# Performance work log

Hardware: AMD Instinct MI355X
Metric: run time of the kernel (lower is better)

Reference implementation:

```python
import jax, jax.numpy as jnp
import numpy as np


def setup_inputs() -> dict:
    key = jax.random.key(0)
    k1, k2, k3 = jax.random.split(key, 3)
    B, C, K, W, H = 8, 512, 512, 64, 64
    x = jax.random.normal(k1, (B, C, W, H), dtype=jnp.float32)
    y = jax.random.normal(k2, (B, K, W, H), dtype=jnp.float32)
    scale = jax.random.uniform(k3, (1,), dtype=jnp.float32)
    return {"x": x, "y": y, "scale": scale}


def reference(x, y, scale):
    B, C, W, H = x.shape
    K = y.shape[1]
    xq = x.reshape(B, C, W * H)            # [B, C, N]
    yk = y.reshape(B, K, W * H)            # [B, K, N]
    # energy = Q @ K^T : [B, C, K]
    energy = jnp.einsum('bcn,bkn->bck', xq, yk)
    # inverted max-subtract softmax over last dim (K)
    energy_new = jnp.max(energy, axis=-1, keepdims=True) - energy
    attention = jax.nn.softmax(energy_new, axis=-1)  # [B, C, K]
    # out = attention @ V : [B, C, N]
    out = jnp.einsum('bck,bkn->bcn', attention, yk).reshape(B, C, W, H)
    return x + scale * out
```

## Files before the change

kernel.cpp:

```cpp
#include <hip/hip_runtime.h>
#include <hip/hip_bf16.h>
#include <stdint.h>

#define BB 8
#define CC 512
#define KK 512
#define NN 4096

typedef __bf16 bf16x8 __attribute__((ext_vector_type(8)));
typedef float f32x4 __attribute__((ext_vector_type(4)));
typedef __attribute__((address_space(3))) uint8_t* lds_ptr_t;
typedef const __attribute__((address_space(1))) uint8_t* gbl_ptr_t;

static __device__ __forceinline__ unsigned short bf16_bits(float f) {
    __bf16 h = (__bf16)f;
    return __builtin_bit_cast(unsigned short, h);
}

__global__ void __launch_bounds__(256) split_hi_lo(const float* __restrict__ in,
        unsigned short* __restrict__ hi, unsigned short* __restrict__ lo, int n4) {
    int idx = blockIdx.x * blockDim.x + threadIdx.x;
    int stride = gridDim.x * blockDim.x;
    const float4* in4 = (const float4*)in;
    ushort4* h4 = (ushort4*)hi;
    ushort4* l4 = (ushort4*)lo;
    for (int i = idx; i < n4; i += stride) {
        float4 v = in4[i];
        float a[4] = {v.x, v.y, v.z, v.w};
        unsigned short hb[4], lb[4];
        #pragma unroll
        for (int j = 0; j < 4; ++j) {
            __bf16 h = (__bf16)a[j];
            float hf = (float)h;
            __bf16 l = (__bf16)(a[j] - hf);
            hb[j] = __builtin_bit_cast(unsigned short, h);
            lb[j] = __builtin_bit_cast(unsigned short, l);
        }
        h4[i] = make_ushort4(hb[0], hb[1], hb[2], hb[3]);
        l4[i] = make_ushort4(lb[0], lb[1], lb[2], lb[3]);
    }
}

__global__ void __launch_bounds__(256) split_y_T(const float* __restrict__ y,
        unsigned short* __restrict__ yh, unsigned short* __restrict__ yl,
        unsigned short* __restrict__ yT) {
    __shared__ unsigned short tile[64][66];
    const int n0 = blockIdx.x * 64, k0 = blockIdx.y * 64, b = blockIdx.z;
    const int t = threadIdx.x;
    const float* src = y + (size_t)b * KK * NN;
    unsigned short* dsth = yh + (size_t)b * KK * NN;
    unsigned short* dstl = yl + (size_t)b * KK * NN;
    unsigned short* dstT = yT + (size_t)b * NN * KK;
    #pragma unroll
    for (int i = 0; i < 4; ++i) {
        int idx = t + 256 * i;
        int r = idx >> 4;
        int c4 = (idx & 15) * 4;
        float4 v = *(const float4*)(src + (size_t)(k0 + r) * NN + n0 + c4);
        float a[4] = {v.x, v.y, v.z, v.w};
        unsigned short hb[4], lb[4];
        #pragma unroll
        for (int q = 0; q < 4; ++q) {
            __bf16 h = (__bf16)a[q];
            float hf = (float)h;
            __bf16 l = (__bf16)(a[q] - hf);
            hb[q] = __builtin_bit_cast(unsigned short, h);
            lb[q] = __builtin_bit_cast(unsigned short, l);
            tile[r][c4 + q] = hb[q];
        }
        size_t off = (size_t)(k0 + r) * NN + n0 + c4;
        *(ushort4*)(dsth + off) = make_ushort4(hb[0], hb[1], hb[2], hb[3]);
        *(ushort4*)(dstl + off) = make_ushort4(lb[0], lb[1], lb[2], lb[3]);
    }
    __syncthreads();
    #pragma unroll
    for (int i = 0; i < 16; ++i) {
        int idx = t + 256 * i;
        int rn = idx >> 6;
        int ck = idx & 63;
        dstT[(size_t)(n0 + rn) * KK + k0 + ck] = tile[ck][rn];
    }
}

__global__ void __launch_bounds__(256) energy_gemm(
        const unsigned short* __restrict__ xh, const unsigned short* __restrict__ xl,
        const unsigned short* __restrict__ yh, const unsigned short* __restrict__ yl,
        float* __restrict__ epart) {
    __shared__ __align__(16) uint8_t smem[4 * 16384];
    const int j = blockIdx.x;
    const int xcd = j & 7;
    const int rem = j >> 3;
    const int ktile = rem & 3;
    const int ctile = (rem >> 2) & 3;
    const int sgrp = rem >> 4;
    const int slice = xcd + 8 * sgrp;
    const int b = slice >> 2;
    const int quarter = slice & 3;
    const int t = threadIdx.x;
    const int wave = t >> 6, lane = t & 63;

    const size_t rowB = (size_t)NN * 2;
    const uint8_t* srcBase[4];
    srcBase[0] = (const uint8_t*)xh + ((size_t)b * CC + ctile * 128) * rowB + (size_t)quarter * 2048;
    srcBase[1] = (const uint8_t*)xl + ((size_t)b * CC + ctile * 128) * rowB + (size_t)quarter * 2048;
    srcBase[2] = (const uint8_t*)yh + ((size_t)b * KK + ktile * 128) * rowB + (size_t)quarter * 2048;
    srcBase[3] = (const uint8_t*)yl + ((size_t)b * KK + ktile * 128) * rowB + (size_t)quarter * 2048;

    f32x4 acc[4][4] = {};
    const int waveRow = wave >> 1, waveCol = wave & 1;

    for (int step = 0; step < 16; ++step) {
        const size_t colByte = (size_t)step * 128;
        #pragma unroll
        for (int i = 0; i < 16; ++i) {
            const int tile = i >> 2;
            const int lc = (i & 3) * 4 + wave;
            const int u = lc * 64 + lane;
            const int r = u >> 3;
            const int c3 = (u & 7) ^ (r & 7);
            const uint8_t* src = srcBase[tile] + (size_t)r * rowB + colByte + c3 * 16;
            __builtin_amdgcn_global_load_lds((gbl_ptr_t)src,
                (lds_ptr_t)(smem + tile * 16384 + lc * 1024), 16, 0, 0);
        }
        __syncthreads();
        #pragma unroll
        for (int kf = 0; kf < 2; ++kf) {
            bf16x8 fah[4], fal[4], fbh[4], fbl[4];
            #pragma unroll
            for (int m = 0; m < 4; ++m) {
                int r = waveRow * 64 + m * 16 + (lane & 15);
                int c3 = (kf * 4 + (lane >> 4)) ^ (r & 7);
                fah[m] = *(const bf16x8*)(smem + 0 * 16384 + r * 128 + c3 * 16);
                fal[m] = *(const bf16x8*)(smem + 1 * 16384 + r * 128 + c3 * 16);
            }
            #pragma unroll
            for (int n = 0; n < 4; ++n) {
                int r = waveCol * 64 + n * 16 + (lane & 15);
                int c3 = (kf * 4 + (lane >> 4)) ^ (r & 7);
                fbh[n] = *(const bf16x8*)(smem + 2 * 16384 + r * 128 + c3 * 16);
                fbl[n] = *(const bf16x8*)(smem + 3 * 16384 + r * 128 + c3 * 16);
            }
            #pragma unroll
            for (int m = 0; m < 4; ++m)
            #pragma unroll
            for (int n = 0; n < 4; ++n) {
                acc[m][n] = __builtin_amdgcn_mfma_f32_16x16x32_bf16(fah[m], fbh[n], acc[m][n], 0, 0, 0);
                acc[m][n] = __builtin_amdgcn_mfma_f32_16x16x32_bf16(fah[m], fbl[n], acc[m][n], 0, 0, 0);
                acc[m][n] = __builtin_amdgcn_mfma_f32_16x16x32_bf16(fal[m], fbh[n], acc[m][n], 0, 0, 0);
            }
        }
        __syncthreads();
    }

    float* eout = epart + (size_t)quarter * BB * CC * KK + (size_t)b * CC * KK;
    const int row0 = ctile * 128 + waveRow * 64;
    const int col0 = ktile * 128 + waveCol * 64;
    #pragma unroll
    for (int m = 0; m < 4; ++m)
    #pragma unroll
    for (int n = 0; n < 4; ++n)
    #pragma unroll
    for (int jj = 0; jj < 4; ++jj) {
        int rr = row0 + m * 16 + (lane >> 4) * 4 + jj;
        int cc2 = col0 + n * 16 + (lane & 15);
        eout[(size_t)rr * KK + cc2] = acc[m][n][jj];
    }
}

__global__ void __launch_bounds__(256) softmax_inv(
        const float* __restrict__ e, unsigned short* __restrict__ att) {
    const int t = threadIdx.x;
    const int wave = t >> 6, lane = t & 63;
    const int row = blockIdx.x * 4 + wave;
    const size_t Q = (size_t)BB * CC * KK;
    const float* p0 = e + (size_t)row * KK;
    float v[8];
    float mn = 3.0e38f;
    #pragma unroll
    for (int i = 0; i < 8; ++i) {
        int c = lane + i * 64;
        v[i] = p0[c] + p0[Q + c] + p0[2 * Q + c] + p0[3 * Q + c];
        mn = fminf(mn, v[i]);
    }
    #pragma unroll
    for (int off = 32; off > 0; off >>= 1) mn = fminf(mn, __shfl_xor(mn, off));
    float p[8]; float s = 0.f;
    #pragma unroll
    for (int i = 0; i < 8; ++i) { p[i] = __expf(mn - v[i]); s += p[i]; }
    #pragma unroll
    for (int off = 32; off > 0; off >>= 1) s += __shfl_xor(s, off);
    float inv = 1.0f / s;
    unsigned short* arow = att + (size_t)row * KK;
    #pragma unroll
    for (int i = 0; i < 8; ++i) arow[lane + i * 64] = bf16_bits(p[i] * inv);
}

__global__ void __launch_bounds__(256) pv_residual(
        const unsigned short* __restrict__ att, const unsigned short* __restrict__ yT,
        const float* __restrict__ x, const float* __restrict__ scale,
        float* __restrict__ out) {
    __shared__ __align__(16) uint8_t smem[2 * 16384];
    const int j = blockIdx.x;
    const int b = j & 7;
    const int rem2 = j >> 3;
    const int ntile = rem2 & 31;
    const int ctile = rem2 >> 5;
    const int t = threadIdx.x;
    const int wave = t >> 6, lane = t & 63;
    const size_t rowB = (size_t)KK * 2;
    const uint8_t* srcA = (const uint8_t*)att + ((size_t)b * CC + ctile * 128) * rowB;
    const uint8_t* srcB = (const uint8_t*)yT  + ((size_t)b * NN + ntile * 128) * rowB;

    f32x4 acc[4][4] = {};
    const int waveRow = wave >> 1, waveCol = wave & 1;

    for (int step = 0; step < 8; ++step) {
        const size_t colByte = (size_t)step * 128;
        #pragma unroll
        for (int i = 0; i < 8; ++i) {
            const uint8_t* base = (i < 4) ? srcA : srcB;
            const int tile = i >> 2;
            const int lc = (i & 3) * 4 + wave;
            const int u = lc * 64 + lane;
            const int r = u >> 3;
            const int c3 = (u & 7) ^ (r & 7);
            const uint8_t* src = base + (size_t)r * rowB + colByte + c3 * 16;
            __builtin_amdgcn_global_load_lds((gbl_ptr_t)src,
                (lds_ptr_t)(smem + tile * 16384 + lc * 1024), 16, 0, 0);
        }
        __syncthreads();
        #pragma unroll
        for (int kf = 0; kf < 2; ++kf) {
            bf16x8 fa[4], fb[4];
            #pragma unroll
            for (int m = 0; m < 4; ++m) {
                int r = waveRow * 64 + m * 16 + (lane & 15);
                int c3 = (kf * 4 + (lane >> 4)) ^ (r & 7);
                fa[m] = *(const bf16x8*)(smem + r * 128 + c3 * 16);
            }
            #pragma unroll
            for (int n = 0; n < 4; ++n) {
                int r = waveCol * 64 + n * 16 + (lane & 15);
                int c3 = (kf * 4 + (lane >> 4)) ^ (r & 7);
                fb[n] = *(const bf16x8*)(smem + 16384 + r * 128 + c3 * 16);
            }
            #pragma unroll
            for (int m = 0; m < 4; ++m)
            #pragma unroll
            for (int n = 0; n < 4; ++n)
                acc[m][n] = __builtin_amdgcn_mfma_f32_16x16x32_bf16(fa[m], fb[n], acc[m][n], 0, 0, 0);
        }
        __syncthreads();
    }

    const float s = scale[0];
    const int row0 = ctile * 128 + waveRow * 64;
    const int col0 = ntile * 128 + waveCol * 64;
    #pragma unroll
    for (int m = 0; m < 4; ++m)
    #pragma unroll
    for (int n = 0; n < 4; ++n)
    #pragma unroll
    for (int jj = 0; jj < 4; ++jj) {
        int rr = row0 + m * 16 + (lane >> 4) * 4 + jj;
        int cc2 = col0 + n * 16 + (lane & 15);
        size_t idx = ((size_t)b * CC + rr) * NN + cc2;
        out[idx] = x[idx] + s * acc[m][n][jj];
    }
}

extern "C" void kernel_launch(void* const* d_in, const int* in_sizes, int n_in,
                              void* d_out, int out_size, void* d_ws, size_t ws_size,
                              hipStream_t stream) {
    const float* x = (const float*)d_in[0];
    const float* y = (const float*)d_in[1];
    const float* scale = (const float*)d_in[2];
    float* out = (float*)d_out;
    uint8_t* ws = (uint8_t*)d_ws;
    uint8_t* ob = (uint8_t*)d_out;
    const size_t MB = 1024 * 1024;
    unsigned short* xh = (unsigned short*)(ws + 0 * MB);
    unsigned short* yh = (unsigned short*)(ws + 32 * MB);
    unsigned short* yl = (unsigned short*)(ws + 64 * MB);
    unsigned short* yT = (unsigned short*)(ws + 96 * MB);
    unsigned short* att = (unsigned short*)(ws + 128 * MB);
    float* epart = (float*)(ob + 0 * MB);
    unsigned short* xl = (unsigned short*)(ob + 32 * MB);

    const int n4 = BB * CC * NN / 4;
    split_hi_lo<<<4096, 256, 0, stream>>>(x, xh, xl, n4);
    split_y_T<<<dim3(NN / 64, KK / 64, BB), 256, 0, stream>>>(y, yh, yl, yT);
    energy_gemm<<<512, 256, 0, stream>>>(xh, xl, yh, yl, epart);
    softmax_inv<<<BB * CC / 4, 256, 0, stream>>>(epart, att);
    pv_residual<<<1024, 256, 0, stream>>>(att, yT, x, scale, out);
}
```

Baseline: 294.1 us.

## Fuse x and y split kernels, simplify energy grid, vectorize softmax

Merges the separate x hi/lo split and y split/transpose kernels into one prep launch, using blockIdx.z to pick x or y work, which removes one launch and lets both run concurrently. The energy GEMM drops its XCD-aware block swizzle in favour of a plain 3D grid, which may change how L2 locality falls across XCDs. The softmax kernel now reads partial energies as float4 and writes attention as ushort4 to cut the number of memory instructions.

```diff
diff --git a/kernel.cpp b/kernel.cpp
--- a/kernel.cpp
+++ b/kernel.cpp
@@ -17,68 +17,74 @@
     return __builtin_bit_cast(unsigned short, h);
 }
 
-__global__ void __launch_bounds__(256) split_hi_lo(const float* __restrict__ in,
-        unsigned short* __restrict__ hi, unsigned short* __restrict__ lo, int n4) {
-    int idx = blockIdx.x * blockDim.x + threadIdx.x;
-    int stride = gridDim.x * blockDim.x;
-    const float4* in4 = (const float4*)in;
-    ushort4* h4 = (ushort4*)hi;
-    ushort4* l4 = (ushort4*)lo;
-    for (int i = idx; i < n4; i += stride) {
-        float4 v = in4[i];
-        float a[4] = {v.x, v.y, v.z, v.w};
-        unsigned short hb[4], lb[4];
-        #pragma unroll
-        for (int j = 0; j < 4; ++j) {
-            __bf16 h = (__bf16)a[j];
-            float hf = (float)h;
-            __bf16 l = (__bf16)(a[j] - hf);
-            hb[j] = __builtin_bit_cast(unsigned short, h);
-            lb[j] = __builtin_bit_cast(unsigned short, l);
-        }
-        h4[i] = make_ushort4(hb[0], hb[1], hb[2], hb[3]);
-        l4[i] = make_ushort4(lb[0], lb[1], lb[2], lb[3]);
-    }
-}
-
-__global__ void __launch_bounds__(256) split_y_T(const float* __restrict__ y,
+__global__ void __launch_bounds__(256) prep(const float* __restrict__ x,
+        const float* __restrict__ y,
+        unsigned short* __restrict__ xh, unsigned short* __restrict__ xl,
         unsigned short* __restrict__ yh, unsigned short* __restrict__ yl,
         unsigned short* __restrict__ yT) {
     __shared__ unsigned short tile[64][66];
-    const int n0 = blockIdx.x * 64, k0 = blockIdx.y * 64, b = blockIdx.z;
+    const int n0 = blockIdx.x * 64, k0 = blockIdx.y * 64;
     const int t = threadIdx.x;
-    const float* src = y + (size_t)b * KK * NN;
-    unsigned short* dsth = yh + (size_t)b * KK * NN;
-    unsigned short* dstl = yl + (size_t)b * KK * NN;
-    unsigned short* dstT = yT + (size_t)b * NN * KK;
-    #pragma unroll
-    for (int i = 0; i < 4; ++i) {
-        int idx = t + 256 * i;
-        int r = idx >> 4;
-        int c4 = (idx & 15) * 4;
-        float4 v = *(const float4*)(src + (size_t)(k0 + r) * NN + n0 + c4);
-        float a[4] = {v.x, v.y, v.z, v.w};
-        unsigned short hb[4], lb[4];
-        #pragma unroll
-        for (int q = 0; q < 4; ++q) {
-            __bf16 h = (__bf16)a[q];
-            float hf = (float)h;
-            __bf16 l = (__bf16)(a[q] - hf);
-            hb[q] = __builtin_bit_cast(unsigned short, h);
-            lb[q] = __builtin_bit_cast(unsigned short, l);
-            tile[r][c4 + q] = hb[q];
-        }
-        size_t off = (size_t)(k0 + r) * NN + n0 + c4;
-        *(ushort4*)(dsth + off) = make_ushort4(hb[0], hb[1], hb[2], hb[3]);
-        *(ushort4*)(dstl + off) = make_ushort4(lb[0], lb[1], lb[2], lb[3]);
-    }
-    __syncthreads();
-    #pragma unroll
-    for (int i = 0; i < 16; ++i) {
-        int idx = t + 256 * i;
-        int rn = idx >> 6;
-        int ck = idx & 63;
-        dstT[(size_t)(n0 + rn) * KK + k0 + ck] = tile[ck][rn];
+    if (blockIdx.z < 8) {
+        const int b = blockIdx.z;
+        const float* src = y + (size_t)b * KK * NN;
+        unsigned short* dsth = yh + (size_t)b * KK * NN;
+        unsigned short* dstl = yl + (size_t)b * KK * NN;
+        unsigned short* dstT = yT + (size_t)b * NN * KK;
+        #pragma unroll
+        for (int i = 0; i < 4; ++i) {
+            int idx = t + 256 * i;
+            int r = idx >> 4;
+            int c4 = (idx & 15) * 4;
+            float4 v = *(const float4*)(src + (size_t)(k0 + r) * NN + n0 + c4);
+            float a[4] = {v.x, v.y, v.z, v.w};
+            unsigned short hb[4], lb[4];
+            #pragma unroll
+            for (int q = 0; q < 4; ++q) {
+                __bf16 h = (__bf16)a[q];
+                float hf = (float)h;
+                __bf16 l = (__bf16)(a[q] - hf);
+                hb[q] = __builtin_bit_cast(unsigned short, h);
+                lb[q] = __builtin_bit_cast(unsigned short, l);
+                tile[r][c4 + q] = hb[q];
+            }
+            size_t off = (size_t)(k0 + r) * NN + n0 + c4;
+            *(ushort4*)(dsth + off) = make_ushort4(hb[0], hb[1], hb[2], hb[3]);
+            *(ushort4*)(dstl + off) = make_ushort4(lb[0], lb[1], lb[2], lb[3]);
+        }
+        __syncthreads();
+        #pragma unroll
+        for (int i = 0; i < 16; ++i) {
+            int idx = t + 256 * i;
+            int rn = idx >> 6;
+            int ck = idx & 63;
+            dstT[(size_t)(n0 + rn) * KK + k0 + ck] = tile[ck][rn];
+        }
+    } else {
+        const int b = blockIdx.z - 8;
+        const float* src = x + (size_t)b * CC * NN;
+        unsigned short* dsth = xh + (size_t)b * CC * NN;
+        unsigned short* dstl = xl + (size_t)b * CC * NN;
+        #pragma unroll
+        for (int i = 0; i < 4; ++i) {
+            int idx = t + 256 * i;
+            int r = idx >> 4;
+            int c4 = (idx & 15) * 4;
+            float4 v = *(const float4*)(src + (size_t)(k0 + r) * NN + n0 + c4);
+            float a[4] = {v.x, v.y, v.z, v.w};
+            unsigned short hb[4], lb[4];
+            #pragma unroll
+            for (int q = 0; q < 4; ++q) {
+                __bf16 h = (__bf16)a[q];
+                float hf = (float)h;
+                __bf16 l = (__bf16)(a[q] - hf);
+                hb[q] = __builtin_bit_cast(unsigned short, h);
+                lb[q] = __builtin_bit_cast(unsigned short, l);
+            }
+            size_t off = (size_t)(k0 + r) * NN + n0 + c4;
+            *(ushort4*)(dsth + off) = make_ushort4(hb[0], hb[1], hb[2], hb[3]);
+            *(ushort4*)(dstl + off) = make_ushort4(lb[0], lb[1], lb[2], lb[3]);
+        }
     }
 }
 
@@ -87,15 +93,10 @@
         const unsigned short* __restrict__ yh, const unsigned short* __restrict__ yl,
         float* __restrict__ epart) {
     __shared__ __align__(16) uint8_t smem[4 * 16384];
-    const int j = blockIdx.x;
-    const int xcd = j & 7;
-    const int rem = j >> 3;
-    const int ktile = rem & 3;
-    const int ctile = (rem >> 2) & 3;
-    const int sgrp = rem >> 4;
-    const int slice = xcd + 8 * sgrp;
-    const int b = slice >> 2;
-    const int quarter = slice & 3;
+    const int ktile = blockIdx.x;
+    const int ctile = blockIdx.y;
+    const int b = blockIdx.z >> 2;
+    const int quarter = blockIdx.z & 3;
     const int t = threadIdx.x;
     const int wave = t >> 6, lane = t & 63;
 
@@ -172,27 +173,35 @@
     const int t = threadIdx.x;
     const int wave = t >> 6, lane = t & 63;
     const int row = blockIdx.x * 4 + wave;
-    const size_t Q = (size_t)BB * CC * KK;
-    const float* p0 = e + (size_t)row * KK;
-    float v[8];
+    const size_t Q4 = (size_t)BB * CC * KK / 4;
+    const f32x4* p = (const f32x4*)(e) + (size_t)row * (KK / 4);
+    f32x4 v[2];
     float mn = 3.0e38f;
     #pragma unroll
-    for (int i = 0; i < 8; ++i) {
+    for (int i = 0; i < 2; ++i) {
         int c = lane + i * 64;
-        v[i] = p0[c] + p0[Q + c] + p0[2 * Q + c] + p0[3 * Q + c];
-        mn = fminf(mn, v[i]);
+        v[i] = p[c] + p[Q4 + c] + p[2 * Q4 + c] + p[3 * Q4 + c];
+        #pragma unroll
+        for (int q = 0; q < 4; ++q) mn = fminf(mn, v[i][q]);
     }
     #pragma unroll
     for (int off = 32; off > 0; off >>= 1) mn = fminf(mn, __shfl_xor(mn, off));
-    float p[8]; float s = 0.f;
-    #pragma unroll
-    for (int i = 0; i < 8; ++i) { p[i] = __expf(mn - v[i]); s += p[i]; }
+    float s = 0.f;
+    f32x4 pr[2];
+    #pragma unroll
+    for (int i = 0; i < 2; ++i)
+    #pragma unroll
+    for (int q = 0; q < 4; ++q) { pr[i][q] = __expf(mn - v[i][q]); s += pr[i][q]; }
     #pragma unroll
     for (int off = 32; off > 0; off >>= 1) s += __shfl_xor(s, off);
     float inv = 1.0f / s;
-    unsigned short* arow = att + (size_t)row * KK;
-    #pragma unroll
-    for (int i = 0; i < 8; ++i) arow[lane + i * 64] = bf16_bits(p[i] * inv);
+    ushort4* arow = (ushort4*)(att + (size_t)row * KK);
+    #pragma unroll
+    for (int i = 0; i < 2; ++i) {
+        arow[lane + i * 64] = make_ushort4(
+            bf16_bits(pr[i][0] * inv), bf16_bits(pr[i][1] * inv),
+            bf16_bits(pr[i][2] * inv), bf16_bits(pr[i][3] * inv));
+    }
 }
 
 __global__ void __launch_bounds__(256) pv_residual(
@@ -287,10 +296,8 @@
     float* epart = (float*)(ob + 0 * MB);
     unsigned short* xl = (unsigned short*)(ob + 32 * MB);
 
-    const int n4 = BB * CC * NN / 4;
-    split_hi_lo<<<4096, 256, 0, stream>>>(x, xh, xl, n4);
-    split_y_T<<<dim3(NN / 64, KK / 64, BB), 256, 0, stream>>>(y, yh, yl, yT);
-    energy_gemm<<<512, 256, 0, stream>>>(xh, xl, yh, yl, epart);
+    prep<<<dim3(NN / 64, KK / 64, 16), 256, 0, stream>>>(x, y, xh, xl, yh, yl, yT);
+    energy_gemm<<<dim3(4, 4, BB * 4), 256, 0, stream>>>(xh, xl, yh, yl, epart);
     softmax_inv<<<BB * CC / 4, 256, 0, stream>>>(epart, att);
     pv_residual<<<1024, 256, 0, stream>>>(att, yT, x, scale, out);
 }
```

Result: no change. 290.6 us (-1.2%).
